# Kernel optimization log

Hardware: AMD Instinct MI355X
Metric: run time of the kernel (lower is better)

Reference implementation:

```python
import jax, jax.numpy as jnp
import numpy as np

K = 2            # kernel_size
NQ = K * K       # 4 qubits
DEPTH = 1


def _apply1(state, U, q):
    # state: (N,2,2,2,2) complex; apply 2x2 gate U on qubit q
    s = jnp.moveaxis(state, 1 + q, -1)
    s = s @ U.T
    return jnp.moveaxis(s, -1, 1 + q)


def _cnot(state, c, t):
    s = jnp.moveaxis(state, (1 + c, 1 + t), (-2, -1))  # (...,2c,2t)
    s = jnp.stack([s[..., 0, :], s[..., 1, ::-1]], axis=-2)
    return jnp.moveaxis(s, (-2, -1), (1 + c, 1 + t))


def _rx(w):
    c, s = jnp.cos(w / 2), jnp.sin(w / 2)
    return jnp.array([[1, 0], [0, 1]], jnp.complex64) * c + jnp.array([[0, -1j], [-1j, 0]], jnp.complex64) * s


def _ry(w):
    c, s = jnp.cos(w / 2), jnp.sin(w / 2)
    return jnp.array([[1, 0], [0, 1]], jnp.complex64) * c + jnp.array([[0, -1], [1, 0]], jnp.complex64) * s


def setup_inputs() -> dict:
    key = jax.random.key(0)
    k1, k2, k3 = jax.random.split(key, 3)
    B, C, H = 1024, 1, 28
    F = H - K + 1
    n_feat = NQ * C * F * F  # 2916
    x = jax.random.uniform(k1, (B, C, H, H), dtype=jnp.float32)
    W = jax.random.normal(k2, (10, n_feat), dtype=jnp.float32)
    b = jax.random.normal(k3, (10,), dtype=jnp.float32)
    weights = jnp.zeros((DEPTH, NQ), dtype=jnp.float32)  # forward() uses zeros, not the Parameter
    return {"x": x, "W": W, "b": b, "weights": weights}


def reference(x, W, b, weights):
    B, C, H, _ = x.shape
    F = H - K + 1
    # extract all KxK patches, row-major within the patch (matches img[c,i:i+k,j:j+k].reshape(-1))
    p = jnp.stack([x[:, :, i:i + F, j:j + F] for i in range(K) for j in range(K)], axis=-1)  # (B,C,F,F,4)
    ang = p.reshape(-1, NQ) * jnp.pi  # AngleEmbedding angles, (N,4)
    # product state from per-qubit RY(theta)|0> = [cos(t/2), sin(t/2)]
    a = jnp.stack([jnp.cos(ang / 2), jnp.sin(ang / 2)], axis=-1).astype(jnp.complex64)  # (N,4,2)
    state = jnp.einsum('na,nb,nc,nd->nabcd', a[:, 0], a[:, 1], a[:, 2], a[:, 3])
    for l in range(DEPTH):
        w = weights[l]
        state = _apply1(state, _rx(w[0]), 0)
        state = _apply1(state, _rx(w[1]), 1)
        state = _cnot(state, 2, 3)
        state = _cnot(state, 0, 2)
        state = _cnot(state, 0, 3)
        state = _apply1(state, _ry(w[2]), 0)
        state = _apply1(state, _ry(w[3]), 3)
    probs = state.real ** 2 + state.imag ** 2  # (N,2,2,2,2)
    z = jnp.array([1.0, -1.0], dtype=x.dtype)
    evs = []
    for q in range(NQ):
        axes = tuple(ax for ax in range(1, 5) if ax != 1 + q)
        evs.append(probs.sum(axes) @ z)  # <Z_q>, (N,)
    evs = jnp.stack(evs, axis=-1)  # (N, 4)
    # per-image reorder: (C*F*F, 4) -> transpose -> (4*C, F, F)
    q = evs.reshape(B, C, F, F, NQ)
    q = jnp.transpose(q, (0, 4, 1, 2, 3)).reshape(B, NQ * C * F * F)
    return q @ W.T + b
```

## Files before the change

kernel.cpp:

```cpp
#include <hip/hip_runtime.h>


#define HD 28
#define NPIX 784
#define FD 27
#define NPATCH 729
#define NF 2916
#define NG 729
#define NOUT 10
#define PSTR 257
#define IM 2

__global__ __launch_bounds__(256)
void hqnn_fused(const float* __restrict__ x,
                const float* __restrict__ W,
                const float* __restrict__ bias,
                const float* __restrict__ wts,
                float* __restrict__ out)
{
    __shared__ __align__(16) float evl[IM][NF];
    __shared__ union U {
        struct { float sc[IM][NPIX]; float ss[IM][NPIX]; } tr;
        float part[IM * NOUT][PSTR];
    } u;

    const int tid = threadIdx.x;

    const float w0 = wts[0], w1 = wts[1], w2 = wts[2], w3 = wts[3];
    const float cw0 = cosf(w0);
    const float cw1 = cosf(w1);
    const float cw2 = cosf(w2), sw2 = sinf(w2);
    const float cw3 = cosf(w3), sw3 = sinf(w3);

    const float4* xb4 = (const float4*)(x + blockIdx.x * (IM * NPIX));
    for (int t = tid; t < IM * NPIX / 4; t += 256) {
        const float4 v = xb4[t];
        const int p4  = t * 4;
        const int img = (p4 >= NPIX) ? 1 : 0;
        const int off = p4 - img * NPIX;
        float s0, c0, s1, c1, s2, c2, s3, c3;
        sincospif(v.x, &s0, &c0);
        sincospif(v.y, &s1, &c1);
        sincospif(v.z, &s2, &c2);
        sincospif(v.w, &s3, &c3);
        u.tr.sc[img][off]     = c0; u.tr.ss[img][off]     = s0;
        u.tr.sc[img][off + 1] = c1; u.tr.ss[img][off + 1] = s1;
        u.tr.sc[img][off + 2] = c2; u.tr.ss[img][off + 2] = s2;
        u.tr.sc[img][off + 3] = c3; u.tr.ss[img][off + 3] = s3;
    }
    __syncthreads();

    for (int pp = tid; pp < IM * NPATCH; pp += 256) {
        const int img = pp / NPATCH;
        const int pa  = pp - img * NPATCH;
        const int fi  = pa / FD;
        const int fj  = pa - fi * FD;
        const int p   = fi * HD + fj;

        const float c00 = u.tr.sc[img][p];
        const float c01 = u.tr.sc[img][p + 1];
        const float c10 = u.tr.sc[img][p + HD];
        const float c11 = u.tr.sc[img][p + HD + 1];
        const float s00 = u.tr.ss[img][p];
        const float s10 = u.tr.ss[img][p + HD];
        const float s11 = u.tr.ss[img][p + HD + 1];

        const float ev2 = cw0 * c00 * c10;
        evl[img][pa]               = cw2 * cw0 * c00 - sw2 * s00 * s10;
        evl[img][NPATCH + pa]      = cw1 * c01;
        evl[img][2 * NPATCH + pa]  = ev2;
        evl[img][3 * NPATCH + pa]  = cw3 * ev2 * c11 - sw3 * s11;
    }
    __syncthreads();

    float acc[IM][NOUT];
#pragma unroll
    for (int m = 0; m < IM; ++m)
#pragma unroll
        for (int o = 0; o < NOUT; ++o) acc[m][o] = 0.f;

    const float4* W4 = (const float4*)W;
    const float4* e0 = (const float4*)evl[0];
    const float4* e1 = (const float4*)evl[1];
    for (int g = tid; g < NG; g += 256) {
        const float4 a = e0[g];
        const float4 c = e1[g];
#pragma unroll
        for (int o = 0; o < NOUT; ++o) {
            const float4 w = W4[o * NG + g];
            acc[0][o] += a.x * w.x + a.y * w.y + a.z * w.z + a.w * w.w;
            acc[1][o] += c.x * w.x + c.y * w.y + c.z * w.z + c.w * w.w;
        }
    }

#pragma unroll
    for (int m = 0; m < IM; ++m)
#pragma unroll
        for (int o = 0; o < NOUT; ++o) u.part[m * NOUT + o][tid] = acc[m][o];
    __syncthreads();

    if (tid < IM * NOUT * 8) {
        const int row = tid >> 3;
        const int j   = tid & 7;
        float s = 0.f;
#pragma unroll
        for (int k = 0; k < 256; k += 8) s += u.part[row][j + k];
        s += __shfl_down(s, 4, 8);
        s += __shfl_down(s, 2, 8);
        s += __shfl_down(s, 1, 8);
        if (j == 0) {
            const int img = (row >= NOUT) ? 1 : 0;
            const int o   = row - img * NOUT;
            out[(blockIdx.x * IM + img) * NOUT + o] = s + bias[o];
        }
    }
}

extern "C" void kernel_launch(void* const* d_in, const int* in_sizes, int n_in,
                              void* d_out, int out_size, void* d_ws, size_t ws_size,
                              hipStream_t stream) {
    const float* x    = (const float*)d_in[0];
    const float* W    = (const float*)d_in[1];
    const float* bias = (const float*)d_in[2];
    const float* wts  = (const float*)d_in[3];
    float* out = (float*)d_out;

    const int B = in_sizes[0] / NPIX;
    hqnn_fused<<<B / IM, 256, 0, stream>>>(x, W, bias, wts, out);
}
```

Baseline: 65.29 us.

## Use 512-thread blocks, prefetch W early, and reduce partials via wave shuffles

Blocks grow from 256 to 512 threads, so each thread handles a single float4 of input and at most two feature groups. The first W chunk and the input are loaded before the trig and patch phases so their global latency overlaps that compute. The shared-memory partial-sum table is replaced by wave-level xor shuffles plus a small per-wave array, and the sin/cos stores become vectorized float4 writes. This cuts loop overhead and LDS traffic, at the cost of more registers held live across barriers (ten prefetched float4 W values) and possibly fewer resident blocks.

```diff
diff --git a/kernel.cpp b/kernel.cpp
--- a/kernel.cpp
+++ b/kernel.cpp
@@ -8,10 +8,11 @@
 #define NF 2916
 #define NG 729
 #define NOUT 10
-#define PSTR 257
 #define IM 2
+#define NT 512
+#define NW (NT / 64)
 
-__global__ __launch_bounds__(256)
+__global__ __launch_bounds__(NT, 4)
 void hqnn_fused(const float* __restrict__ x,
                 const float* __restrict__ W,
                 const float* __restrict__ bias,
@@ -19,12 +20,22 @@
                 float* __restrict__ out)
 {
     __shared__ __align__(16) float evl[IM][NF];
-    __shared__ union U {
-        struct { float sc[IM][NPIX]; float ss[IM][NPIX]; } tr;
-        float part[IM * NOUT][PSTR];
-    } u;
+    __shared__ __align__(16) float sc[IM][NPIX];
+    __shared__ __align__(16) float ss[IM][NPIX];
+    __shared__ float wsum[NW][IM * NOUT];
 
     const int tid = threadIdx.x;
+
+    const float4* xb4 = (const float4*)(x + (size_t)blockIdx.x * (IM * NPIX));
+    const bool hasx = tid < (IM * NPIX / 4);
+    float4 v;
+    if (hasx) v = xb4[tid];
+
+    const float4* W4 = (const float4*)W;
+    const int g0 = tid;
+    float4 wA[NOUT];
+#pragma unroll
+    for (int o = 0; o < NOUT; ++o) wA[o] = W4[o * NG + g0];
 
     const float w0 = wts[0], w1 = wts[1], w2 = wts[2], w3 = wts[3];
     const float cw0 = cosf(w0);
@@ -32,10 +43,8 @@
     const float cw2 = cosf(w2), sw2 = sinf(w2);
     const float cw3 = cosf(w3), sw3 = sinf(w3);
 
-    const float4* xb4 = (const float4*)(x + blockIdx.x * (IM * NPIX));
-    for (int t = tid; t < IM * NPIX / 4; t += 256) {
-        const float4 v = xb4[t];
-        const int p4  = t * 4;
+    if (hasx) {
+        const int p4  = tid * 4;
         const int img = (p4 >= NPIX) ? 1 : 0;
         const int off = p4 - img * NPIX;
         float s0, c0, s1, c1, s2, c2, s3, c3;
@@ -43,27 +52,25 @@
         sincospif(v.y, &s1, &c1);
         sincospif(v.z, &s2, &c2);
         sincospif(v.w, &s3, &c3);
-        u.tr.sc[img][off]     = c0; u.tr.ss[img][off]     = s0;
-        u.tr.sc[img][off + 1] = c1; u.tr.ss[img][off + 1] = s1;
-        u.tr.sc[img][off + 2] = c2; u.tr.ss[img][off + 2] = s2;
-        u.tr.sc[img][off + 3] = c3; u.tr.ss[img][off + 3] = s3;
+        *(float4*)&sc[img][off] = make_float4(c0, c1, c2, c3);
+        *(float4*)&ss[img][off] = make_float4(s0, s1, s2, s3);
     }
     __syncthreads();
 
-    for (int pp = tid; pp < IM * NPATCH; pp += 256) {
-        const int img = pp / NPATCH;
+    for (int pp = tid; pp < IM * NPATCH; pp += NT) {
+        const int img = (pp >= NPATCH) ? 1 : 0;
         const int pa  = pp - img * NPATCH;
         const int fi  = pa / FD;
         const int fj  = pa - fi * FD;
         const int p   = fi * HD + fj;
 
-        const float c00 = u.tr.sc[img][p];
-        const float c01 = u.tr.sc[img][p + 1];
-        const float c10 = u.tr.sc[img][p + HD];
-        const float c11 = u.tr.sc[img][p + HD + 1];
-        const float s00 = u.tr.ss[img][p];
-        const float s10 = u.tr.ss[img][p + HD];
-        const float s11 = u.tr.ss[img][p + HD + 1];
+        const float c00 = sc[img][p];
+        const float c01 = sc[img][p + 1];
+        const float c10 = sc[img][p + HD];
+        const float c11 = sc[img][p + HD + 1];
+        const float s00 = ss[img][p];
+        const float s10 = ss[img][p + HD];
+        const float s11 = ss[img][p + HD + 1];
 
         const float ev2 = cw0 * c00 * c10;
         evl[img][pa]               = cw2 * cw0 * c00 - sw2 * s00 * s10;
@@ -73,46 +80,55 @@
     }
     __syncthreads();
 
-    float acc[IM][NOUT];
-#pragma unroll
-    for (int m = 0; m < IM; ++m)
-#pragma unroll
-        for (int o = 0; o < NOUT; ++o) acc[m][o] = 0.f;
-
-    const float4* W4 = (const float4*)W;
     const float4* e0 = (const float4*)evl[0];
     const float4* e1 = (const float4*)evl[1];
-    for (int g = tid; g < NG; g += 256) {
-        const float4 a = e0[g];
-        const float4 c = e1[g];
+    float acc[IM][NOUT];
+    {
+        const float4 a = e0[g0];
+        const float4 c = e1[g0];
 #pragma unroll
         for (int o = 0; o < NOUT; ++o) {
-            const float4 w = W4[o * NG + g];
+            const float4 w = wA[o];
+            acc[0][o] = a.x * w.x + a.y * w.y + a.z * w.z + a.w * w.w;
+            acc[1][o] = c.x * w.x + c.y * w.y + c.z * w.z + c.w * w.w;
+        }
+    }
+    const int g1 = tid + NT;
+    if (g1 < NG) {
+        const float4 a = e0[g1];
+        const float4 c = e1[g1];
+#pragma unroll
+        for (int o = 0; o < NOUT; ++o) {
+            const float4 w = W4[o * NG + g1];
             acc[0][o] += a.x * w.x + a.y * w.y + a.z * w.z + a.w * w.w;
             acc[1][o] += c.x * w.x + c.y * w.y + c.z * w.z + c.w * w.w;
         }
     }
 
+    const int wv = tid >> 6;
+    const int ln = tid & 63;
 #pragma unroll
     for (int m = 0; m < IM; ++m)
 #pragma unroll
-        for (int o = 0; o < NOUT; ++o) u.part[m * NOUT + o][tid] = acc[m][o];
+        for (int o = 0; o < NOUT; ++o) {
+            float s = acc[m][o];
+            s += __shfl_xor(s, 32);
+            s += __shfl_xor(s, 16);
+            s += __shfl_xor(s, 8);
+            s += __shfl_xor(s, 4);
+            s += __shfl_xor(s, 2);
+            s += __shfl_xor(s, 1);
+            if (ln == 0) wsum[wv][m * NOUT + o] = s;
+        }
     __syncthreads();
 
-    if (tid < IM * NOUT * 8) {
-        const int row = tid >> 3;
-        const int j   = tid & 7;
+    if (tid < IM * NOUT) {
         float s = 0.f;
 #pragma unroll
-        for (int k = 0; k < 256; k += 8) s += u.part[row][j + k];
-        s += __shfl_down(s, 4, 8);
-        s += __shfl_down(s, 2, 8);
-        s += __shfl_down(s, 1, 8);
-        if (j == 0) {
-            const int img = (row >= NOUT) ? 1 : 0;
-            const int o   = row - img * NOUT;
-            out[(blockIdx.x * IM + img) * NOUT + o] = s + bias[o];
-        }
+        for (int w = 0; w < NW; ++w) s += wsum[w][tid];
+        const int img = (tid >= NOUT) ? 1 : 0;
+        const int o   = tid - img * NOUT;
+        out[(blockIdx.x * IM + img) * NOUT + o] = s + bias[o];
     }
 }
 
@@ -126,5 +142,5 @@
     float* out = (float*)d_out;
 
     const int B = in_sizes[0] / NPIX;
-    hqnn_fused<<<B / IM, 256, 0, stream>>>(x, W, bias, wts, out);
+    hqnn_fused<<<B / IM, NT, 0, stream>>>(x, W, bias, wts, out);
 }
```

Result: slower. 68.91 us (+5.5%).
